# Optimization experiments

Hardware: AMD Instinct MI355X
Metric: run time of the kernel (lower is better)

Reference implementation:

```python
import jax, jax.numpy as jnp
import numpy as np

N_IN, D_IN, N_OUT, D_OUT = 1152, 8, 10, 16
ROUTINGS, NUM_BG = 3, 1
C, H, W = 1, 28, 28
BATCH = 128
DEC_IN = N_OUT * D_OUT  # 160, projection_type=None -> dec_feature_size = outcaps_size


def squash(x, axis=-1):
    norm = jnp.linalg.norm(x, axis=axis, keepdims=True)
    scale = norm ** 2 / (1.0 + norm ** 2) / (norm + 1e-8)
    return scale * x


def scale_coef(x, num_bg):
    # x: [B, n_out] or [B, n_out, n_in]; min/max normalize over dim 1,
    # excluding the last num_bg (background) capsules, then floor at 0.5.
    if num_bg > 0:
        xm = x[:, : x.shape[1] - num_bg]
    else:
        xm = x
    mn = jnp.min(xm, axis=1, keepdims=True)
    mx = jnp.max(xm, axis=1, keepdims=True)
    out = (xm - mn) / jnp.maximum(mx - mn, 1e-6)  # vrange (0,1)
    if num_bg > 0:
        out = jnp.concatenate([out, jnp.zeros_like(out[:, :num_bg])], axis=1)
    return jnp.maximum(out, 0.5)


def decode(capsflat, W1, b1, W2, b2, W3, b3):
    # fcn decoder (eval mode: dropout is identity): 160 -> 512 -> 1024 -> C*H*W
    h = jax.nn.relu(capsflat @ W1 + b1)
    h = jax.nn.relu(h @ W2 + b2)
    return jax.nn.sigmoid(h @ W3 + b3)


def setup_inputs() -> dict:
    key = jax.random.key(0)
    ks = jax.random.split(key, 9)
    return {
        'incaps': jax.random.normal(ks[0], (BATCH, N_IN, D_IN), jnp.float32),
        'x_input': jax.random.uniform(ks[1], (BATCH, C, H, W), jnp.float32),
        'weight': 0.1 * jax.random.normal(ks[2], (N_OUT, N_IN, D_OUT, D_IN), jnp.float32),
        'W1': 0.05 * jax.random.normal(ks[3], (DEC_IN, 512), jnp.float32),
        'b1': jnp.zeros((512,), jnp.float32),
        'W2': 0.05 * jax.random.normal(ks[4], (512, 1024), jnp.float32),
        'b2': jnp.zeros((1024,), jnp.float32),
        'W3': 0.05 * jax.random.normal(ks[5], (1024, C * H * W), jnp.float32),
        'b3': jnp.zeros((C * H * W,), jnp.float32),
    }


def reference(incaps, x_input, weight, W1, b1, W2, b2, W3, b3):
    B = incaps.shape[0]
    # outcaps_hat: matmul(weight, incaps[:,None,:,:,None]).squeeze(-1)
    hat = jnp.einsum('nkoi,bki->bnko', weight, incaps)  # [B, n_out, n_in, d_out]
    hat_d = jax.lax.stop_gradient(hat)
    rc = jnp.ones((B, N_OUT, N_IN), hat.dtype)
    eye = jnp.eye(N_OUT, dtype=hat.dtype)
    x_flat = x_input.reshape(B, 1, -1)
    for _ in range(ROUTINGS - 1):
        # squash over capsule dim, weighted sum over input capsules
        outcaps = squash(jnp.sum(rc[..., None] * hat_d, axis=2, keepdims=True))  # [B,n,1,d]
        b = jnp.sum(outcaps * hat_d, axis=-1)  # agreement [B, n_out, n_in]
        c = scale_coef(b, NUM_BG)
        objcaps = outcaps[:, :, 0, :]  # [B, n_out, d_out]
        # get_every_obj_rscore vectorized: mask one object capsule at a time
        masked = objcaps[:, None, :, :] * eye[None, :, :, None]  # [B, n_obj, n_out, d]
        recon = decode(masked.reshape(B, N_OUT, DEC_IN), W1, b1, W2, b2, W3, b3)  # [B,n_obj,CHW]
        rscore = -jnp.sum((x_flat - recon) ** 2, axis=-1)  # neg MSE-sum, [B, n_obj]
        r = scale_coef(rscore, NUM_BG)
        rc = c * r[:, :, None]
    # final iteration uses non-detached hat
    outcaps = squash(jnp.sum(rc[..., None] * hat, axis=2, keepdims=True))
    return outcaps[:, :, 0, :]  # [B, n_out, d_out]
```

## Files before the change

### kernel.cpp

```cpp
#include <hip/hip_runtime.h>
#include <math.h>

#define BATCH  128
#define NIN    1152
#define DIN    8
#define NOUTC  10
#define DOUT   16
#define H1DIM  512
#define H2DIM  1024
#define PIX    784
#define NROWS  (BATCH * NOUTC)
#define NBY3   13

typedef __attribute__((ext_vector_type(8))) __bf16 bf16x8;
typedef __attribute__((ext_vector_type(4))) float  f32x4;

__device__ __forceinline__ float bf2f(unsigned int u) {
    union { unsigned int i; float f; } v; v.i = u << 16; return v.f;
}
__device__ __forceinline__ ushort f2bf(float f) {
    union { float f; unsigned int i; } v; v.f = f;
    unsigned int r = v.i + 0x7FFFu + ((v.i >> 16) & 1u);
    return (ushort)(r >> 16);
}
__device__ __forceinline__ float ldin(const void* p, size_t i, int isbf) {
    return isbf ? bf2f(((const ushort*)p)[i]) : ((const float*)p)[i];
}
__device__ __forceinline__ bf16x8 ld_frag(const ushort* p) {
    uint4 u = *(const uint4*)p;
    return __builtin_bit_cast(bf16x8, u);
}
__device__ __forceinline__ float dot8(uint4 a, uint4 b) {
    float s;
    s  = bf2f(a.x & 0xffffu) * bf2f(b.x & 0xffffu);
    s += bf2f(a.x >> 16)     * bf2f(b.x >> 16);
    s += bf2f(a.y & 0xffffu) * bf2f(b.y & 0xffffu);
    s += bf2f(a.y >> 16)     * bf2f(b.y >> 16);
    s += bf2f(a.z & 0xffffu) * bf2f(b.z & 0xffffu);
    s += bf2f(a.z >> 16)     * bf2f(b.z >> 16);
    s += bf2f(a.w & 0xffffu) * bf2f(b.w & 0xffffu);
    s += bf2f(a.w >> 16)     * bf2f(b.w >> 16);
    return s;
}

struct PrepArgs {
    const void* src[9];
    ushort*     dst[9];
    int         n[9];
    int*        flag;
};

__global__ __launch_bounds__(256) void prep_kernel(PrepArgs a)
{
    __shared__ int cntS;
    __shared__ ushort tile[32][33];
    int tid = threadIdx.x;
    if (tid == 0) cntS = 0;
    __syncthreads();
    {
        const ushort* wu = (const ushort*)a.src[0];
        int c = 0;
        for (int s = tid; s < 512; s += 256) {
            int e = (wu[s * 2] >> 7) & 0xFF;
            if (e >= 88 && e <= 140) c++;
        }
        atomicAdd(&cntS, c);
    }
    __syncthreads();
    int isbf = (cntS >= 384) ? 1 : 0;
    int seg = blockIdx.y;
    if (seg == 0 && blockIdx.x == 0 && tid == 0) *a.flag = isbf;

    if (seg <= 6) {
        int n = a.n[seg];
        int stride = gridDim.x * 256;
        ushort* d = a.dst[seg];
        if (isbf) {
            const ushort* s = (const ushort*)a.src[seg];
            for (int i = blockIdx.x * 256 + tid; i < n; i += stride) d[i] = s[i];
        } else {
            const float* s = (const float*)a.src[seg];
            for (int i = blockIdx.x * 256 + tid; i < n; i += stride) d[i] = f2bf(s[i]);
        }
        return;
    }
    int R = (seg == 7) ? H1DIM : H2DIM;
    int C = (seg == 7) ? H2DIM : PIX;
    int tilesX = (seg == 7) ? 32 : 25;
    int tilesY = (seg == 7) ? 16 : 32;
    int t = blockIdx.x;
    if (t >= tilesX * tilesY) return;
    int tx2 = t % tilesX, ty2 = t / tilesX;
    int c0 = tx2 * 32, r0 = ty2 * 32;
    const void* in = a.src[seg];
    ushort* out = a.dst[seg];
    int tx = tid & 31, ty = tid >> 5;
    for (int i = ty; i < 32; i += 8) {
        int r = r0 + i, c = c0 + tx;
        tile[i][tx] = (r < R && c < C) ? f2bf(ldin(in, (size_t)r * C + c, isbf)) : (ushort)0;
    }
    __syncthreads();
    for (int i = ty; i < 32; i += 8) {
        int c = c0 + i, r = r0 + tx;
        if (c < C && r < R) out[(size_t)c * R + r] = tile[tx][i];
    }
}

__global__ __launch_bounds__(256) void hat_build(
    const ushort* __restrict__ icvt,
    const ushort* __restrict__ wcvt,
    ushort* __restrict__ hatG)
{
    int kc = blockIdx.x, bc = blockIdx.y, n = blockIdx.z;
    int t  = threadIdx.x;
    int k  = kc * 128 + (t >> 1);
    int oh = (t & 1) << 3;

    const uint4* wp = (const uint4*)(wcvt + (((size_t)n * NIN + k) * DOUT + oh) * DIN);
    uint4 wr[8];
    #pragma unroll
    for (int j = 0; j < 8; j++) wr[j] = wp[j];

    int b0 = bc * 16;
    #pragma unroll 4
    for (int bl = 0; bl < 16; bl++) {
        int b = b0 + bl;
        uint4 iu = *(const uint4*)(icvt + ((size_t)b * NIN + k) * DIN);
        unsigned int h[8];
        #pragma unroll
        for (int j = 0; j < 8; j++) h[j] = f2bf(dot8(wr[j], iu));
        uint4 ov;
        ov.x = h[0] | (h[1] << 16);
        ov.y = h[2] | (h[3] << 16);
        ov.z = h[4] | (h[5] << 16);
        ov.w = h[6] | (h[7] << 16);
        *(uint4*)(hatG + (((size_t)(b * NOUTC + n) * NIN + k) * DOUT + oh)) = ov;
    }
}

template<bool COMPUTE>
__global__ __launch_bounds__(256) void reduce_pass(
    const ushort* __restrict__ hatG,
    const ushort* __restrict__ icvt,
    const ushort* __restrict__ wcvt,
    const ushort* __restrict__ bsPrev,
    const float*  __restrict__ partials,
    int iter0,
    float*  __restrict__ outcapsWS,
    const ushort* __restrict__ W1c,
    const ushort* __restrict__ b1c,
    ushort* __restrict__ h1out,
    ushort* __restrict__ bsOut,
    void*   __restrict__ outFinal,
    const int* __restrict__ flagp)
{
    int bn  = blockIdx.x;
    int n   = bn % NOUTC;
    int b   = bn / NOUTC;
    int tid = threadIdx.x;

    __shared__ uint4  hatS4[NIN * DOUT / 8];
    __shared__ ushort wSb[NIN];
    __shared__ float  redS[4][16];
    __shared__ float  sumS[16];
    __shared__ float  ocS[16];
    __shared__ float  scaleS;
    ushort* hatS = (ushort*)hatS4;

    if constexpr (COMPUTE) {
        __shared__ uint4 incS4[NIN * DIN / 8];
        const uint4* incp = (const uint4*)(icvt + (size_t)b * NIN * DIN);
        for (int i = tid; i < NIN * DIN / 8; i += 256) incS4[i] = incp[i];
        if (!iter0) {
            float v[9], mn = 1e30f, mx = -1e30f;
            #pragma unroll
            for (int n2 = 0; n2 < 9; n2++) {
                float s = 0.f;
                for (int j = 0; j < NBY3; j++)
                    s += partials[(size_t)(b * NOUTC + n2) * 16 + j];
                v[n2] = -s;
                mn = fminf(mn, v[n2]); mx = fmaxf(mx, v[n2]);
            }
            float den = fmaxf(mx - mn, 1e-6f);
            float rv = (n < 9) ? fmaxf((v[n] - mn) / den, 0.5f) : 0.5f;
            for (int k = tid; k < NIN; k += 256) {
                float c = 0.5f;
                if (n < 9) {
                    float vv[9], mn2 = 1e30f, mx2 = -1e30f;
                    #pragma unroll
                    for (int n2 = 0; n2 < 9; n2++) {
                        vv[n2] = bf2f(bsPrev[(size_t)(b * NOUTC + n2) * NIN + k]);
                        mn2 = fminf(mn2, vv[n2]); mx2 = fmaxf(mx2, vv[n2]);
                    }
                    float den2 = fmaxf(mx2 - mn2, 1e-6f);
                    c = fmaxf((vv[n] - mn2) / den2, 0.5f);
                }
                wSb[k] = f2bf(c * rv);
            }
        }
        __syncthreads();
        const ushort* incS = (const ushort*)incS4;
        const ushort* wp = wcvt + (size_t)n * NIN * DOUT * DIN;
        for (int idx = tid; idx < NIN * DOUT; idx += 256) {
            int k = idx >> 4;
            uint4 wu = *(const uint4*)(wp + (size_t)idx * 8);
            uint4 iu = *(const uint4*)(incS + k * 8);
            hatS[idx] = f2bf(dot8(wu, iu));
        }
        __syncthreads();
    } else {
        const uint4* hp = (const uint4*)(hatG + (size_t)bn * NIN * DOUT);
        #pragma unroll
        for (int i = 0; i < 9; i++) hatS4[tid + 256 * i] = hp[tid + 256 * i];
        if (!iter0) {
            float v[9], mn = 1e30f, mx = -1e30f;
            #pragma unroll
            for (int n2 = 0; n2 < 9; n2++) {
                float s = 0.f;
                for (int j = 0; j < NBY3; j++)
                    s += partials[(size_t)(b * NOUTC + n2) * 16 + j];
                v[n2] = -s;
                mn = fminf(mn, v[n2]); mx = fmaxf(mx, v[n2]);
            }
            float den = fmaxf(mx - mn, 1e-6f);
            float rv = (n < 9) ? fmaxf((v[n] - mn) / den, 0.5f) : 0.5f;
            for (int k = tid; k < NIN; k += 256) {
                float c = 0.5f;
                if (n < 9) {
                    float vv[9], mn2 = 1e30f, mx2 = -1e30f;
                    #pragma unroll
                    for (int n2 = 0; n2 < 9; n2++) {
                        vv[n2] = bf2f(bsPrev[(size_t)(b * NOUTC + n2) * NIN + k]);
                        mn2 = fminf(mn2, vv[n2]); mx2 = fmaxf(mx2, vv[n2]);
                    }
                    float den2 = fmaxf(mx2 - mn2, 1e-6f);
                    c = fmaxf((vv[n] - mn2) / den2, 0.5f);
                }
                wSb[k] = f2bf(c * rv);
            }
        }
        __syncthreads();
    }

    int h = tid & 1, kb = tid >> 1;
    int wave = tid >> 6, lane = tid & 63;
    float acc[8];
    #pragma unroll
    for (int o = 0; o < 8; o++) acc[o] = 0.f;
    #pragma unroll
    for (int j = 0; j < 9; j++) {
        int k = kb + 128 * j;
        float w = iter0 ? 1.f : bf2f(wSb[k]);
        bf16x8 hv = ld_frag(hatS + k * 16 + h * 8);
        #pragma unroll
        for (int o = 0; o < 8; o++) acc[o] += w * (float)hv[o];
    }
    #pragma unroll
    for (int off = 32; off >= 2; off >>= 1) {
        #pragma unroll
        for (int o = 0; o < 8; o++) acc[o] += __shfl_xor(acc[o], off);
    }
    if (lane < 2) {
        #pragma unroll
        for (int o = 0; o < 8; o++) redS[wave][lane * 8 + o] = acc[o];
    }
    __syncthreads();
    if (tid < 16)
        sumS[tid] = redS[0][tid] + redS[1][tid] + redS[2][tid] + redS[3][tid];
    __syncthreads();
    if (tid == 0) {
        float n2 = 0.f;
        #pragma unroll
        for (int o = 0; o < 16; o++) n2 += sumS[o] * sumS[o];
        float nrm = sqrtf(n2);
        scaleS = n2 / (1.f + n2) / (nrm + 1e-8f);
    }
    __syncthreads();
    if (tid < 16) {
        float oc = scaleS * sumS[tid];
        ocS[tid] = oc;
        outcapsWS[(size_t)bn * 16 + tid] = oc;
        if (outFinal) {
            if (*flagp) ((ushort*)outFinal)[(size_t)bn * 16 + tid] = f2bf(oc);
            else        ((float*) outFinal)[(size_t)bn * 16 + tid] = oc;
        }
    }
    __syncthreads();

    if (bsOut) {
        #pragma unroll
        for (int j = 0; j < 9; j++) {
            int k = kb + 128 * j;
            bf16x8 hv = ld_frag(hatS + k * 16 + h * 8);
            float s = 0.f;
            #pragma unroll
            for (int o = 0; o < 8; o++) s += ocS[h * 8 + o] * (float)hv[o];
            s += __shfl_xor(s, 1);
            if (h == 0) bsOut[(size_t)bn * NIN + k] = f2bf(s);
        }
    }

    if (h1out) {
        for (int col = tid; col < H1DIM; col += 256) {
            float acc1 = bf2f(b1c[col]);
            #pragma unroll
            for (int i = 0; i < 16; i++)
                acc1 += ocS[i] * bf2f(W1c[(size_t)(n * 16 + i) * H1DIM + col]);
            h1out[(size_t)bn * H1DIM + col] = f2bf(fmaxf(acc1, 0.f));
        }
    }
}

__global__ __launch_bounds__(256) void gemm_kernel(
    const ushort* __restrict__ A, const ushort* __restrict__ Bt,
    const ushort* __restrict__ bias, int K, int N,
    ushort* __restrict__ Cout,
    const ushort* __restrict__ xin, float* __restrict__ partials)
{
    int m0 = blockIdx.x * 64, n0 = blockIdx.y * 64;
    int tid = threadIdx.x;
    int wave = tid >> 6, lane = tid & 63, quad = lane >> 4, l16 = lane & 15;

    __shared__ uint4 As4[256];
    __shared__ uint4 Bs4[256];
    ushort* As = (ushort*)As4;
    ushort* Bs = (ushort*)Bs4;

    f32x4 acc[4];
    #pragma unroll
    for (int nt = 0; nt < 4; nt++)
        #pragma unroll
        for (int rg = 0; rg < 4; rg++) acc[nt][rg] = 0.f;

    int sMi = tid >> 2, sKk = (tid & 3) * 8;
    const ushort* Ap = A + (size_t)(m0 + sMi) * K + sKk;
    const ushort* Bp = Bt + (size_t)(n0 + sMi) * K + sKk;
    bool bOK = (n0 + sMi) < N;

    uint4 aR = *(const uint4*)Ap;
    uint4 bR = bOK ? *(const uint4*)Bp : make_uint4(0, 0, 0, 0);

    for (int k0 = 0; k0 < K; k0 += 32) {
        As4[tid] = aR;
        Bs4[tid] = bR;
        __syncthreads();
        if (k0 + 32 < K) {
            aR = *(const uint4*)(Ap + k0 + 32);
            bR = bOK ? *(const uint4*)(Bp + k0 + 32) : make_uint4(0, 0, 0, 0);
        }
        bf16x8 a = ld_frag(As + (wave * 16 + l16) * 32 + quad * 8);
        #pragma unroll
        for (int nt = 0; nt < 4; nt++) {
            bf16x8 bb = ld_frag(Bs + (nt * 16 + l16) * 32 + quad * 8);
            acc[nt] = __builtin_amdgcn_mfma_f32_16x16x32_bf16(a, bb, acc[nt], 0, 0, 0);
        }
        __syncthreads();
    }

    int rowBase = m0 + wave * 16 + quad * 4;
    if (Cout) {
        #pragma unroll
        for (int nt = 0; nt < 4; nt++) {
            int col = n0 + nt * 16 + l16;
            float bv = bf2f(bias[col]);
            #pragma unroll
            for (int rg = 0; rg < 4; rg++) {
                float v = acc[nt][rg] + bv;
                Cout[(size_t)(rowBase + rg) * N + col] = f2bf(fmaxf(v, 0.f));
            }
        }
    } else {
        float vr[4] = {0.f, 0.f, 0.f, 0.f};
        #pragma unroll
        for (int nt = 0; nt < 4; nt++) {
            int col = n0 + nt * 16 + l16;
            if (col < N) {
                float bv = bf2f(bias[col]);
                #pragma unroll
                for (int rg = 0; rg < 4; rg++) {
                    int row = rowBase + rg;
                    int bb = row / NOUTC;
                    float z = acc[nt][rg] + bv;
                    float s = 1.f / (1.f + __expf(-z));
                    float d = bf2f(xin[(size_t)bb * PIX + col]) - s;
                    vr[rg] += d * d;
                }
            }
        }
        #pragma unroll
        for (int rg = 0; rg < 4; rg++) {
            float v = vr[rg];
            #pragma unroll
            for (int off = 8; off >= 1; off >>= 1) v += __shfl_xor(v, off, 16);
            if (l16 == 0)
                partials[(size_t)(rowBase + rg) * 16 + blockIdx.y] = v;
        }
    }
}

extern "C" void kernel_launch(void* const* d_in, const int* in_sizes, int n_in,
                              void* d_out, int out_size, void* d_ws, size_t ws_size,
                              hipStream_t stream)
{
    const void* inc = d_in[0];
    const void* x   = d_in[1];
    const void* w   = d_in[2];
    const void* W1  = d_in[3];
    const void* b1  = d_in[4];
    const void* W2  = d_in[5];
    const void* b2  = d_in[6];
    const void* W3  = d_in[7];
    const void* b3  = d_in[8];

    char* p = (char*)d_ws;
    auto alloc = [&](size_t bytes) { void* r = p; p += (bytes + 255) & ~(size_t)255; return r; };
    int*    flagWS    = (int*)alloc(256);
    float*  outcapsWS = (float*)alloc((size_t)NROWS * 16 * 4);
    ushort* bsA       = (ushort*)alloc((size_t)NROWS * NIN * 2);
    ushort* bsB       = (ushort*)alloc((size_t)NROWS * NIN * 2);
    float*  partials  = (float*)alloc((size_t)NROWS * 16 * 4);
    ushort* h1WS      = (ushort*)alloc((size_t)NROWS * H1DIM * 2);
    ushort* h2WS      = (ushort*)alloc((size_t)NROWS * H2DIM * 2);
    ushort* W2T       = (ushort*)alloc((size_t)H2DIM * H1DIM * 2);
    ushort* W3T       = (ushort*)alloc((size_t)PIX * H2DIM * 2);
    ushort* wcvt      = (ushort*)alloc((size_t)NOUTC * NIN * DOUT * DIN * 2);
    ushort* icvt      = (ushort*)alloc((size_t)BATCH * NIN * DIN * 2);
    ushort* W1c       = (ushort*)alloc((size_t)160 * H1DIM * 2);
    ushort* b1c       = (ushort*)alloc((size_t)H1DIM * 2);
    ushort* b2c       = (ushort*)alloc((size_t)H2DIM * 2);
    ushort* b3c       = (ushort*)alloc((size_t)PIX * 2);
    ushort* xc        = (ushort*)alloc((size_t)BATCH * PIX * 2);
    ushort* hatG      = (ushort*)alloc((size_t)NROWS * NIN * DOUT * 2);
    bool haveHat = ((char*)hatG + (size_t)NROWS * NIN * DOUT * 2) <= ((char*)d_ws + ws_size);

    PrepArgs pa;
    pa.src[0] = w;   pa.dst[0] = wcvt; pa.n[0] = NOUTC * NIN * DOUT * DIN;
    pa.src[1] = inc; pa.dst[1] = icvt; pa.n[1] = BATCH * NIN * DIN;
    pa.src[2] = W1;  pa.dst[2] = W1c;  pa.n[2] = 160 * H1DIM;
    pa.src[3] = b1;  pa.dst[3] = b1c;  pa.n[3] = H1DIM;
    pa.src[4] = b2;  pa.dst[4] = b2c;  pa.n[4] = H2DIM;
    pa.src[5] = b3;  pa.dst[5] = b3c;  pa.n[5] = PIX;
    pa.src[6] = x;   pa.dst[6] = xc;   pa.n[6] = BATCH * PIX;
    pa.src[7] = W2;  pa.dst[7] = W2T;  pa.n[7] = 0;
    pa.src[8] = W3;  pa.dst[8] = W3T;  pa.n[8] = 0;
    pa.flag = flagWS;
    prep_kernel<<<dim3(800, 9), 256, 0, stream>>>(pa);

    if (haveHat) hat_build<<<dim3(9, 8, NOUTC), 256, 0, stream>>>(icvt, wcvt, hatG);

    if (haveHat)
        reduce_pass<false><<<NROWS, 256, 0, stream>>>(
            hatG, icvt, wcvt, nullptr, nullptr, 1, outcapsWS,
            W1c, b1c, h1WS, bsA, nullptr, flagWS);
    else
        reduce_pass<true><<<NROWS, 256, 0, stream>>>(
            nullptr, icvt, wcvt, nullptr, nullptr, 1, outcapsWS,
            W1c, b1c, h1WS, bsA, nullptr, flagWS);

    for (int it = 0; it < 2; it++) {
        gemm_kernel<<<dim3(NROWS / 64, H2DIM / 64), 256, 0, stream>>>(
            h1WS, W2T, b2c, H1DIM, H2DIM, h2WS, nullptr, nullptr);
        gemm_kernel<<<dim3(NROWS / 64, NBY3), 256, 0, stream>>>(
            h2WS, W3T, b3c, H2DIM, PIX, nullptr, xc, partials);

        int last = (it == 1);
        const ushort* bsP = (it == 0) ? bsA : bsB;
        ushort* bsO       = last ? nullptr : bsB;
        ushort* h1o       = last ? nullptr : h1WS;
        void*   fin       = last ? d_out : nullptr;
        if (haveHat)
            reduce_pass<false><<<NROWS, 256, 0, stream>>>(
                hatG, icvt, wcvt, bsP, partials, 0, outcapsWS,
                W1c, b1c, h1o, bsO, fin, flagWS);
        else
            reduce_pass<true><<<NROWS, 256, 0, stream>>>(
                nullptr, icvt, wcvt, bsP, partials, 0, outcapsWS,
                W1c, b1c, h1o, bsO, fin, flagWS);
    }
}
```

Before: 229.9 us.

## Widen reduce_pass to 512 threads, pad GEMM LDS, use nontemporal hat traffic

The reduce pass now runs 512 threads per block. The partials sum is done by 9 threads and shared through LDS instead of being recomputed by every thread, and the duplicated routing-coefficient code is merged. The GEMM LDS tiles are padded to a 40-element row stride to avoid bank conflicts. The hat tensor is written and read with nontemporal stores and loads to reduce cache pollution, and the unused outcaps workspace write is dropped. The larger blocks add barrier cost, and the nontemporal hints could hurt if the hat data would otherwise have been reused from L2.

```diff
diff --git a/kernel.cpp b/kernel.cpp
--- a/kernel.cpp
+++ b/kernel.cpp
@@ -14,6 +14,7 @@
 
 typedef __attribute__((ext_vector_type(8))) __bf16 bf16x8;
 typedef __attribute__((ext_vector_type(4))) float  f32x4;
+typedef __attribute__((ext_vector_type(4))) unsigned int u32x4;
 
 __device__ __forceinline__ float bf2f(unsigned int u) {
     union { unsigned int i; float f; } v; v.i = u << 16; return v.f;
@@ -129,24 +130,21 @@
         unsigned int h[8];
         #pragma unroll
         for (int j = 0; j < 8; j++) h[j] = f2bf(dot8(wr[j], iu));
-        uint4 ov;
-        ov.x = h[0] | (h[1] << 16);
-        ov.y = h[2] | (h[3] << 16);
-        ov.z = h[4] | (h[5] << 16);
-        ov.w = h[6] | (h[7] << 16);
-        *(uint4*)(hatG + (((size_t)(b * NOUTC + n) * NIN + k) * DOUT + oh)) = ov;
+        u32x4 ov = { h[0] | (h[1] << 16), h[2] | (h[3] << 16),
+                     h[4] | (h[5] << 16), h[6] | (h[7] << 16) };
+        __builtin_nontemporal_store(ov,
+            (u32x4*)(hatG + (((size_t)(b * NOUTC + n) * NIN + k) * DOUT + oh)));
     }
 }
 
 template<bool COMPUTE>
-__global__ __launch_bounds__(256) void reduce_pass(
+__global__ __launch_bounds__(512, 8) void reduce_pass(
     const ushort* __restrict__ hatG,
     const ushort* __restrict__ icvt,
     const ushort* __restrict__ wcvt,
     const ushort* __restrict__ bsPrev,
     const float*  __restrict__ partials,
     int iter0,
-    float*  __restrict__ outcapsWS,
     const ushort* __restrict__ W1c,
     const ushort* __restrict__ b1c,
     ushort* __restrict__ h1out,
@@ -161,7 +159,7 @@
 
     __shared__ uint4  hatS4[NIN * DOUT / 8];
     __shared__ ushort wSb[NIN];
-    __shared__ float  redS[4][16];
+    __shared__ float  redS[8][16];
     __shared__ float  sumS[16];
     __shared__ float  ocS[16];
     __shared__ float  scaleS;
@@ -170,77 +168,57 @@
     if constexpr (COMPUTE) {
         __shared__ uint4 incS4[NIN * DIN / 8];
         const uint4* incp = (const uint4*)(icvt + (size_t)b * NIN * DIN);
-        for (int i = tid; i < NIN * DIN / 8; i += 256) incS4[i] = incp[i];
-        if (!iter0) {
-            float v[9], mn = 1e30f, mx = -1e30f;
-            #pragma unroll
-            for (int n2 = 0; n2 < 9; n2++) {
-                float s = 0.f;
-                for (int j = 0; j < NBY3; j++)
-                    s += partials[(size_t)(b * NOUTC + n2) * 16 + j];
-                v[n2] = -s;
-                mn = fminf(mn, v[n2]); mx = fmaxf(mx, v[n2]);
-            }
-            float den = fmaxf(mx - mn, 1e-6f);
-            float rv = (n < 9) ? fmaxf((v[n] - mn) / den, 0.5f) : 0.5f;
-            for (int k = tid; k < NIN; k += 256) {
-                float c = 0.5f;
-                if (n < 9) {
-                    float vv[9], mn2 = 1e30f, mx2 = -1e30f;
-                    #pragma unroll
-                    for (int n2 = 0; n2 < 9; n2++) {
-                        vv[n2] = bf2f(bsPrev[(size_t)(b * NOUTC + n2) * NIN + k]);
-                        mn2 = fminf(mn2, vv[n2]); mx2 = fmaxf(mx2, vv[n2]);
-                    }
-                    float den2 = fmaxf(mx2 - mn2, 1e-6f);
-                    c = fmaxf((vv[n] - mn2) / den2, 0.5f);
-                }
-                wSb[k] = f2bf(c * rv);
-            }
-        }
+        for (int i = tid; i < NIN * DIN / 8; i += 512) incS4[i] = incp[i];
         __syncthreads();
         const ushort* incS = (const ushort*)incS4;
         const ushort* wp = wcvt + (size_t)n * NIN * DOUT * DIN;
-        for (int idx = tid; idx < NIN * DOUT; idx += 256) {
+        for (int idx = tid; idx < NIN * DOUT; idx += 512) {
             int k = idx >> 4;
             uint4 wu = *(const uint4*)(wp + (size_t)idx * 8);
             uint4 iu = *(const uint4*)(incS + k * 8);
             hatS[idx] = f2bf(dot8(wu, iu));
         }
+    } else {
+        const u32x4* hp = (const u32x4*)(hatG + (size_t)bn * NIN * DOUT);
+        for (int i = tid; i < NIN * DOUT / 8; i += 512) {
+            u32x4 v = __builtin_nontemporal_load(hp + i);
+            hatS4[i] = __builtin_bit_cast(uint4, v);
+        }
+    }
+
+    if (!iter0) {
+        if (tid < 9) {
+            float s = 0.f;
+            #pragma unroll
+            for (int j = 0; j < NBY3; j++)
+                s += partials[(size_t)(b * NOUTC + tid) * 16 + j];
+            sumS[tid] = -s;
+        }
         __syncthreads();
-    } else {
-        const uint4* hp = (const uint4*)(hatG + (size_t)bn * NIN * DOUT);
-        #pragma unroll
-        for (int i = 0; i < 9; i++) hatS4[tid + 256 * i] = hp[tid + 256 * i];
-        if (!iter0) {
-            float v[9], mn = 1e30f, mx = -1e30f;
-            #pragma unroll
-            for (int n2 = 0; n2 < 9; n2++) {
-                float s = 0.f;
-                for (int j = 0; j < NBY3; j++)
-                    s += partials[(size_t)(b * NOUTC + n2) * 16 + j];
-                v[n2] = -s;
-                mn = fminf(mn, v[n2]); mx = fmaxf(mx, v[n2]);
+        float mn = 1e30f, mx = -1e30f;
+        #pragma unroll
+        for (int n2 = 0; n2 < 9; n2++) {
+            float v = sumS[n2];
+            mn = fminf(mn, v); mx = fmaxf(mx, v);
+        }
+        float den = fmaxf(mx - mn, 1e-6f);
+        float rv = (n < 9) ? fmaxf((sumS[n] - mn) / den, 0.5f) : 0.5f;
+        for (int k = tid; k < NIN; k += 512) {
+            float c = 0.5f;
+            if (n < 9) {
+                float vv[9], mn2 = 1e30f, mx2 = -1e30f;
+                #pragma unroll
+                for (int n2 = 0; n2 < 9; n2++) {
+                    vv[n2] = bf2f(bsPrev[(size_t)(b * NOUTC + n2) * NIN + k]);
+                    mn2 = fminf(mn2, vv[n2]); mx2 = fmaxf(mx2, vv[n2]);
+                }
+                float den2 = fmaxf(mx2 - mn2, 1e-6f);
+                c = fmaxf((vv[n] - mn2) / den2, 0.5f);
             }
-            float den = fmaxf(mx - mn, 1e-6f);
-            float rv = (n < 9) ? fmaxf((v[n] - mn) / den, 0.5f) : 0.5f;
-            for (int k = tid; k < NIN; k += 256) {
-                float c = 0.5f;
-                if (n < 9) {
-                    float vv[9], mn2 = 1e30f, mx2 = -1e30f;
-                    #pragma unroll
-                    for (int n2 = 0; n2 < 9; n2++) {
-                        vv[n2] = bf2f(bsPrev[(size_t)(b * NOUTC + n2) * NIN + k]);
-                        mn2 = fminf(mn2, vv[n2]); mx2 = fmaxf(mx2, vv[n2]);
-                    }
-                    float den2 = fmaxf(mx2 - mn2, 1e-6f);
-                    c = fmaxf((vv[n] - mn2) / den2, 0.5f);
-                }
-                wSb[k] = f2bf(c * rv);
-            }
-        }
-        __syncthreads();
-    }
+            wSb[k] = f2bf(c * rv);
+        }
+    }
+    __syncthreads();
 
     int h = tid & 1, kb = tid >> 1;
     int wave = tid >> 6, lane = tid & 63;
@@ -248,13 +226,20 @@
     #pragma unroll
     for (int o = 0; o < 8; o++) acc[o] = 0.f;
     #pragma unroll
-    for (int j = 0; j < 9; j++) {
-        int k = kb + 128 * j;
+    for (int j = 0; j < 4; j++) {
+        int k = kb + 256 * j;
         float w = iter0 ? 1.f : bf2f(wSb[k]);
         bf16x8 hv = ld_frag(hatS + k * 16 + h * 8);
         #pragma unroll
         for (int o = 0; o < 8; o++) acc[o] += w * (float)hv[o];
     }
+    if (kb < 128) {
+        int k = 1024 + kb;
+        float w = iter0 ? 1.f : bf2f(wSb[k]);
+        bf16x8 hv = ld_frag(hatS + k * 16 + h * 8);
+        #pragma unroll
+        for (int o = 0; o < 8; o++) acc[o] += w * (float)hv[o];
+    }
     #pragma unroll
     for (int off = 32; off >= 2; off >>= 1) {
         #pragma unroll
@@ -265,8 +250,12 @@
         for (int o = 0; o < 8; o++) redS[wave][lane * 8 + o] = acc[o];
     }
     __syncthreads();
-    if (tid < 16)
-        sumS[tid] = redS[0][tid] + redS[1][tid] + redS[2][tid] + redS[3][tid];
+    if (tid < 16) {
+        float s = 0.f;
+        #pragma unroll
+        for (int wv = 0; wv < 8; wv++) s += redS[wv][tid];
+        sumS[tid] = s;
+    }
     __syncthreads();
     if (tid == 0) {
         float n2 = 0.f;
@@ -279,7 +268,6 @@
     if (tid < 16) {
         float oc = scaleS * sumS[tid];
         ocS[tid] = oc;
-        outcapsWS[(size_t)bn * 16 + tid] = oc;
         if (outFinal) {
             if (*flagp) ((ushort*)outFinal)[(size_t)bn * 16 + tid] = f2bf(oc);
             else        ((float*) outFinal)[(size_t)bn * 16 + tid] = oc;
@@ -289,8 +277,8 @@
 
     if (bsOut) {
         #pragma unroll
-        for (int j = 0; j < 9; j++) {
-            int k = kb + 128 * j;
+        for (int j = 0; j < 4; j++) {
+            int k = kb + 256 * j;
             bf16x8 hv = ld_frag(hatS + k * 16 + h * 8);
             float s = 0.f;
             #pragma unroll
@@ -298,16 +286,24 @@
             s += __shfl_xor(s, 1);
             if (h == 0) bsOut[(size_t)bn * NIN + k] = f2bf(s);
         }
+        if (kb < 128) {
+            int k = 1024 + kb;
+            bf16x8 hv = ld_frag(hatS + k * 16 + h * 8);
+            float s = 0.f;
+            #pragma unroll
+            for (int o = 0; o < 8; o++) s += ocS[h * 8 + o] * (float)hv[o];
+            s += __shfl_xor(s, 1);
+            if (h == 0) bsOut[(size_t)bn * NIN + k] = f2bf(s);
+        }
     }
 
     if (h1out) {
-        for (int col = tid; col < H1DIM; col += 256) {
-            float acc1 = bf2f(b1c[col]);
-            #pragma unroll
-            for (int i = 0; i < 16; i++)
-                acc1 += ocS[i] * bf2f(W1c[(size_t)(n * 16 + i) * H1DIM + col]);
-            h1out[(size_t)bn * H1DIM + col] = f2bf(fmaxf(acc1, 0.f));
-        }
+        int col = tid;
+        float acc1 = bf2f(b1c[col]);
+        #pragma unroll
+        for (int i = 0; i < 16; i++)
+            acc1 += ocS[i] * bf2f(W1c[(size_t)(n * 16 + i) * H1DIM + col]);
+        h1out[(size_t)bn * H1DIM + col] = f2bf(fmaxf(acc1, 0.f));
     }
 }
 
@@ -321,8 +317,8 @@
     int tid = threadIdx.x;
     int wave = tid >> 6, lane = tid & 63, quad = lane >> 4, l16 = lane & 15;
 
-    __shared__ uint4 As4[256];
-    __shared__ uint4 Bs4[256];
+    __shared__ uint4 As4[320];
+    __shared__ uint4 Bs4[320];
     ushort* As = (ushort*)As4;
     ushort* Bs = (ushort*)Bs4;
 
@@ -333,6 +329,7 @@
         for (int rg = 0; rg < 4; rg++) acc[nt][rg] = 0.f;
 
     int sMi = tid >> 2, sKk = (tid & 3) * 8;
+    int sLds = sMi * 5 + (tid & 3);
     const ushort* Ap = A + (size_t)(m0 + sMi) * K + sKk;
     const ushort* Bp = Bt + (size_t)(n0 + sMi) * K + sKk;
     bool bOK = (n0 + sMi) < N;
@@ -341,17 +338,17 @@
     uint4 bR = bOK ? *(const uint4*)Bp : make_uint4(0, 0, 0, 0);
 
     for (int k0 = 0; k0 < K; k0 += 32) {
-        As4[tid] = aR;
-        Bs4[tid] = bR;
+        As4[sLds] = aR;
+        Bs4[sLds] = bR;
         __syncthreads();
         if (k0 + 32 < K) {
             aR = *(const uint4*)(Ap + k0 + 32);
             bR = bOK ? *(const uint4*)(Bp + k0 + 32) : make_uint4(0, 0, 0, 0);
         }
-        bf16x8 a = ld_frag(As + (wave * 16 + l16) * 32 + quad * 8);
+        bf16x8 a = ld_frag(As + (wave * 16 + l16) * 40 + quad * 8);
         #pragma unroll
         for (int nt = 0; nt < 4; nt++) {
-            bf16x8 bb = ld_frag(Bs + (nt * 16 + l16) * 32 + quad * 8);
+            bf16x8 bb = ld_frag(Bs + (nt * 16 + l16) * 40 + quad * 8);
             acc[nt] = __builtin_amdgcn_mfma_f32_16x16x32_bf16(a, bb, acc[nt], 0, 0, 0);
         }
         __syncthreads();
@@ -415,7 +412,6 @@
     char* p = (char*)d_ws;
     auto alloc = [&](size_t bytes) { void* r = p; p += (bytes + 255) & ~(size_t)255; return r; };
     int*    flagWS    = (int*)alloc(256);
-    float*  outcapsWS = (float*)alloc((size_t)NROWS * 16 * 4);
     ushort* bsA       = (ushort*)alloc((size_t)NROWS * NIN * 2);
     ushort* bsB       = (ushort*)alloc((size_t)NROWS * NIN * 2);
     float*  partials  = (float*)alloc((size_t)NROWS * 16 * 4);
@@ -449,12 +445,12 @@
     if (haveHat) hat_build<<<dim3(9, 8, NOUTC), 256, 0, stream>>>(icvt, wcvt, hatG);
 
     if (haveHat)
-        reduce_pass<false><<<NROWS, 256, 0, stream>>>(
-            hatG, icvt, wcvt, nullptr, nullptr, 1, outcapsWS,
+        reduce_pass<false><<<NROWS, 512, 0, stream>>>(
+            hatG, icvt, wcvt, nullptr, nullptr, 1,
             W1c, b1c, h1WS, bsA, nullptr, flagWS);
     else
-        reduce_pass<true><<<NROWS, 256, 0, stream>>>(
-            nullptr, icvt, wcvt, nullptr, nullptr, 1, outcapsWS,
+        reduce_pass<true><<<NROWS, 512, 0, stream>>>(
+            nullptr, icvt, wcvt, nullptr, nullptr, 1,
             W1c, b1c, h1WS, bsA, nullptr, flagWS);
 
     for (int it = 0; it < 2; it++) {
@@ -469,12 +465,12 @@
         ushort* h1o       = last ? nullptr : h1WS;
         void*   fin       = last ? d_out : nullptr;
         if (haveHat)
-            reduce_pass<false><<<NROWS, 256, 0, stream>>>(
-                hatG, icvt, wcvt, bsP, partials, 0, outcapsWS,
+            reduce_pass<false><<<NROWS, 512, 0, stream>>>(
+                hatG, icvt, wcvt, bsP, partials, 0,
                 W1c, b1c, h1o, bsO, fin, flagWS);
         else
-            reduce_pass<true><<<NROWS, 256, 0, stream>>>(
-                nullptr, icvt, wcvt, bsP, partials, 0, outcapsWS,
+            reduce_pass<true><<<NROWS, 512, 0, stream>>>(
+                nullptr, icvt, wcvt, bsP, partials, 0,
                 W1c, b1c, h1o, bsO, fin, flagWS);
     }
 }
```

New measurement: 215.3 us. -6.3%, faster.
